# Performance work log

Hardware: AMD Instinct MI355X
Metric: run time of the kernel (lower is better)

Reference implementation:

```python
import jax, jax.numpy as jnp
import numpy as np

S = (256, 256, 256)          # MRI volume shape
N = 50000                    # number of Gaussians
T = 16                       # fixed tile edge; covers max bbox width = 2*3*sigma_max*(S-1)+2 <= 15
SIG_MIN, SIG_MAX = 0.004, 0.008  # NN-distance-based sigma range (k_sigma=1)


def setup_inputs() -> dict:
    key = jax.random.key(0)
    k1, k2, k3 = jax.random.split(key, 3)
    centers = jax.random.uniform(k1, (N, 3), dtype=jnp.float32)
    sigmas = jax.random.uniform(k2, (N,), dtype=jnp.float32, minval=SIG_MIN, maxval=SIG_MAX)
    intensities = jax.random.uniform(k3, (N,), dtype=jnp.float32)
    return {"centers": centers, "sigmas": sigmas, "intensities": intensities}


def _splat(centers, sigmas, intensities):
    dt = centers.dtype
    scale = jnp.asarray([s - 1 for s in S], dtype=dt)            # (3,) == scale_factors
    shape_f = jnp.asarray(S, dtype=dt)                           # (3,)
    shape_i = jnp.asarray(S, dtype=jnp.int32)                    # (3,)

    center_vox = centers * scale                                 # (N,3) voxel-space centers
    cutoff = 3.0 * sigmas[:, None] * scale                       # (N,3)
    # original: min_idx = max(c-cut, 0).int(); max_idx = (min(c+cut, scale)+1).int(), clipped to S
    min_idx = jnp.floor(jnp.maximum(center_vox - cutoff, 0.0)).astype(jnp.int32)          # (N,3)
    max_idx = jnp.minimum(jnp.floor(jnp.minimum(center_vox + cutoff, scale)) + 1.0,
                          shape_f).astype(jnp.int32)             # (N,3), exclusive

    ar = jnp.arange(T, dtype=jnp.int32)
    idx = min_idx[:, :, None] + ar[None, None, :]                # (N,3,T) absolute voxel idx
    valid = idx < max_idx[:, :, None]                            # (N,3,T) inside variable bbox
    idx_c = jnp.minimum(idx, shape_i[None, :, None] - 1)         # clamp for safe gather/scatter

    # grid coordinate along axis a at voxel i is i/(S_a-1) (linspace(0,1,S_a))
    coord = idx_c.astype(dt) / scale[None, :, None]              # (N,3,T)
    d = coord - centers[:, :, None]                              # (N,3,T)
    d2 = (d[:, 0, :, None, None] ** 2
          + d[:, 1, None, :, None] ** 2
          + d[:, 2, None, None, :] ** 2)                         # (N,T,T,T)
    mask = (valid[:, 0, :, None, None]
            & valid[:, 1, None, :, None]
            & valid[:, 2, None, None, :])                        # (N,T,T,T)

    inv_two_sig2 = 0.5 / (sigmas * sigmas)                       # (N,)
    contrib = intensities[:, None, None, None] * jnp.exp(-d2 * inv_two_sig2[:, None, None, None])
    contrib = jnp.where(mask, contrib, jnp.zeros((), dt))        # (N,T,T,T)

    lin = (idx_c[:, 0, :, None, None] * (S[1] * S[2])
           + idx_c[:, 1, None, :, None] * S[2]
           + idx_c[:, 2, None, None, :])                         # (N,T,T,T) flat voxel index

    vol = jnp.zeros(S[0] * S[1] * S[2], dtype=dt)
    vol = vol.at[lin.reshape(-1)].add(contrib.reshape(-1))
    return vol.reshape(S)


def reference(centers, sigmas, intensities):
    return _splat(centers, sigmas, intensities)
```

## Files before the change

kernel.cpp:

```cpp
#include <hip/hip_runtime.h>


#define NTILE  32768
#define CAP    64
#define LOG2E  1.4426950408889634f

__global__ __launch_bounds__(256) void bin_prep_kernel(
    const float* __restrict__ centers,
    const float* __restrict__ sigmas,
    const float* __restrict__ intens,
    int*    __restrict__ counts,
    float4* __restrict__ prep,
    int*    __restrict__ list,
    int N)
{
    int g = blockIdx.x * 256 + threadIdx.x;
    if (g >= N) return;
    float c0 = centers[3*g+0], c1 = centers[3*g+1], c2 = centers[3*g+2];
    float sig = sigmas[g];
    float cut = 3.0f * sig * 255.0f;
    float c[3] = {c0, c1, c2};
    int mn[3], mx[3];
    #pragma unroll
    for (int a = 0; a < 3; ++a) {
        float cv = c[a] * 255.0f;
        mn[a] = (int)floorf(fmaxf(cv - cut, 0.0f));
        mx[a] = (int)fminf(floorf(fminf(cv + cut, 255.0f)) + 1.0f, 256.0f);
    }
    float s255 = sig * 255.0f;
    float w2 = -0.5f * LOG2E / (s255 * s255);
    unsigned mnp = (unsigned)mn[0] | ((unsigned)mn[1] << 10) | ((unsigned)mn[2] << 20);
    unsigned mxp = (unsigned)mx[0] | ((unsigned)mx[1] << 10) | ((unsigned)mx[2] << 20);
    prep[2*g+0] = make_float4(c0 * 255.0f, c1 * 255.0f, c2 * 255.0f, w2);
    prep[2*g+1] = make_float4(intens[g], __uint_as_float(mnp), __uint_as_float(mxp), 0.0f);

    int t0x = mn[0] >> 3, t1x = (mx[0] - 1) >> 3;
    int t0y = mn[1] >> 3, t1y = (mx[1] - 1) >> 3;
    int t0z = mn[2] >> 3, t1z = (mx[2] - 1) >> 3;
    for (int tx = t0x; tx <= t1x; ++tx)
        for (int ty = t0y; ty <= t1y; ++ty)
            for (int tz = t0z; tz <= t1z; ++tz) {
                int t = (tx << 10) | (ty << 5) | tz;
                int slot = atomicAdd(&counts[t], 1);
                if (slot < CAP) list[t * CAP + slot] = g;
            }
}

__global__ __launch_bounds__(256) void splat_main(
    const float4* __restrict__ prep,
    const int*    __restrict__ counts,
    const int*    __restrict__ list,
    float* __restrict__ vol)
{
    int wid = threadIdx.x >> 6;
    int t   = __builtin_amdgcn_readfirstlane(blockIdx.x * 4 + wid);
    int tx = t >> 10, ty = (t >> 5) & 31, tz = t & 31;
    int ox = tx << 3, oy = ty << 3, oz = tz << 3;
    int lane = threadIdx.x & 63;
    int ly = lane >> 3, lz = lane & 7, tap = lane & 7;

    int n    = counts[t]; if (n > CAP) n = CAP;
    int base = t * CAP;

    float fyv = (float)(oy + ly);
    float fzv = (float)(oz + lz);
    float fxv = (float)(ox + tap);

    float acc[8];
    #pragma unroll
    for (int i = 0; i < 8; ++i) acc[i] = 0.0f;

    for (int k = 0; k < n; ++k) {
        int g = __builtin_amdgcn_readfirstlane(list[base + k]);
        float4 p0 = prep[2*g+0];
        float4 p1 = prep[2*g+1];

        unsigned mnp = __float_as_uint(p1.y);
        unsigned mxp = __float_as_uint(p1.z);
        int lox = max((int)( mnp        & 1023) - ox, 0), hix = min((int)( mxp        & 1023) - ox, 8);
        int loy = max((int)((mnp >> 10) & 1023) - oy, 0), hiy = min((int)((mxp >> 10) & 1023) - oy, 8);
        int loz = max((int)((mnp >> 20) & 1023) - oz, 0), hiz = min((int)((mxp >> 20) & 1023) - oz, 8);

        float dy = fyv - p0.y, dz = fzv - p0.z;
        float eyz = exp2f(fmaf(dy, dy, dz * dz) * p0.w) * p1.x;
        bool vyz = (ly >= loy) & (ly < hiy) & (lz >= loz) & (lz < hiz);
        eyz = vyz ? eyz : 0.0f;

        float dx = fxv - p0.x;
        float exv = exp2f(dx * dx * p0.w);
        bool vx = (tap >= lox) & (tap < hix);
        exv = vx ? exv : 0.0f;
        int exb = __float_as_int(exv);

        #pragma unroll
        for (int i = 0; i < 8; ++i) {
            float sx = __int_as_float(__builtin_amdgcn_readlane(exb, i));
            acc[i] = fmaf(sx, eyz, acc[i]);
        }
    }

    int ybase = ((oy + ly) << 8) + (oz + lz);
    #pragma unroll
    for (int i = 0; i < 8; ++i)
        vol[((ox + i) << 16) + ybase] = acc[i];
}

extern "C" void kernel_launch(void* const* d_in, const int* in_sizes, int n_in,
                              void* d_out, int out_size, void* d_ws, size_t ws_size,
                              hipStream_t stream) {
    const float* centers = (const float*)d_in[0];
    const float* sigmas  = (const float*)d_in[1];
    const float* intens  = (const float*)d_in[2];
    float* vol = (float*)d_out;
    const int N = in_sizes[1];

    char* ws = (char*)d_ws;
    int*    counts = (int*)ws;
    float4* prep   = (float4*)(ws + (size_t)NTILE * sizeof(int));
    int*    list   = (int*)(ws + (size_t)NTILE * sizeof(int) + (size_t)N * 32);

    hipMemsetAsync(counts, 0, NTILE * sizeof(int), stream);

    int gblocks = (N + 255) / 256;
    bin_prep_kernel<<<gblocks, 256, 0, stream>>>(centers, sigmas, intens,
                                                 counts, prep, list, N);
    splat_main<<<NTILE / 4, 256, 0, stream>>>(prep, counts, list, vol);
}
```

Measured before the change: 144.2 us.

## Precompute per-tile masks in binning and software-prefetch next Gaussian in splat loop

The binning pass now stores, for each Gaussian-tile pair, an int2 holding the Gaussian index together with precomputed x/z bit patterns and y shift amounts. The splat loop turns these into wave-wide SGPR masks applied with v_cndmask, so the per-lane bounds comparisons disappear. Intensity is folded into the exponent as log2 and added inside exp2, which removes a multiply. The next list entry and its prep data are loaded one iteration ahead to hide load latency, and CAP drops from 64 to 48, which risks overflow on dense tiles and packs the index into 16 bits, so it only works for N below 65536.

After: 141.8 us. About the same (-1.7%).

```diff
diff --git a/kernel.cpp b/kernel.cpp
--- a/kernel.cpp
+++ b/kernel.cpp
@@ -1,9 +1,11 @@
 #include <hip/hip_runtime.h>
 
 
-#define NTILE  32768
-#define CAP    64
-#define LOG2E  1.4426950408889634f
+#define NTILE 32768
+#define CAP   48
+#define LOG2E 1.4426950408889634f
+
+typedef unsigned long long ull;
 
 __global__ __launch_bounds__(256) void bin_prep_kernel(
     const float* __restrict__ centers,
@@ -11,51 +13,60 @@
     const float* __restrict__ intens,
     int*    __restrict__ counts,
     float4* __restrict__ prep,
-    int*    __restrict__ list,
+    int2*   __restrict__ list,
     int N)
 {
     int g = blockIdx.x * 256 + threadIdx.x;
     if (g >= N) return;
-    float c0 = centers[3*g+0], c1 = centers[3*g+1], c2 = centers[3*g+2];
+    float c0 = centers[3*g+0] * 255.0f;
+    float c1 = centers[3*g+1] * 255.0f;
+    float c2 = centers[3*g+2] * 255.0f;
     float sig = sigmas[g];
     float cut = 3.0f * sig * 255.0f;
-    float c[3] = {c0, c1, c2};
+    float cc[3] = {c0, c1, c2};
     int mn[3], mx[3];
     #pragma unroll
     for (int a = 0; a < 3; ++a) {
-        float cv = c[a] * 255.0f;
-        mn[a] = (int)floorf(fmaxf(cv - cut, 0.0f));
-        mx[a] = (int)fminf(floorf(fminf(cv + cut, 255.0f)) + 1.0f, 256.0f);
+        mn[a] = (int)floorf(fmaxf(cc[a] - cut, 0.0f));
+        mx[a] = (int)fminf(floorf(fminf(cc[a] + cut, 255.0f)) + 1.0f, 256.0f);
     }
     float s255 = sig * 255.0f;
     float w2 = -0.5f * LOG2E / (s255 * s255);
-    unsigned mnp = (unsigned)mn[0] | ((unsigned)mn[1] << 10) | ((unsigned)mn[2] << 20);
-    unsigned mxp = (unsigned)mx[0] | ((unsigned)mx[1] << 10) | ((unsigned)mx[2] << 20);
-    prep[2*g+0] = make_float4(c0 * 255.0f, c1 * 255.0f, c2 * 255.0f, w2);
-    prep[2*g+1] = make_float4(intens[g], __uint_as_float(mnp), __uint_as_float(mxp), 0.0f);
+    float b  = log2f(intens[g]);
+    prep[2*g+0] = make_float4(c0, c1, c2, w2);
+    prep[2*g+1] = make_float4(b, 0.0f, 0.0f, 0.0f);
 
     int t0x = mn[0] >> 3, t1x = (mx[0] - 1) >> 3;
     int t0y = mn[1] >> 3, t1y = (mx[1] - 1) >> 3;
     int t0z = mn[2] >> 3, t1z = (mx[2] - 1) >> 3;
-    for (int tx = t0x; tx <= t1x; ++tx)
-        for (int ty = t0y; ty <= t1y; ++ty)
+    for (int tx = t0x; tx <= t1x; ++tx) {
+        int lox = max(mn[0] - (tx << 3), 0), hix = min(mx[0] - (tx << 3), 8);
+        unsigned xpat = (0xFFu >> (8 - hix)) & (0xFFu << lox);
+        for (int ty = t0y; ty <= t1y; ++ty) {
+            int loy = max(mn[1] - (ty << 3), 0), hiy = min(mx[1] - (ty << 3), 8);
+            int s1 = loy << 3, s2 = 64 - (hiy << 3);
             for (int tz = t0z; tz <= t1z; ++tz) {
+                int loz = max(mn[2] - (tz << 3), 0), hiz = min(mx[2] - (tz << 3), 8);
+                unsigned zpat = (0xFFu >> (8 - hiz)) & (0xFFu << loz);
                 int t = (tx << 10) | (ty << 5) | tz;
+                int w0 = g | (int)(xpat << 16);
+                int w1 = (int)(zpat | ((unsigned)s1 << 8) | ((unsigned)s2 << 16));
                 int slot = atomicAdd(&counts[t], 1);
-                if (slot < CAP) list[t * CAP + slot] = g;
+                if (slot < CAP) list[t * CAP + slot] = make_int2(w0, w1);
             }
+        }
+    }
 }
 
 __global__ __launch_bounds__(256) void splat_main(
     const float4* __restrict__ prep,
     const int*    __restrict__ counts,
-    const int*    __restrict__ list,
+    const int2*   __restrict__ list,
     float* __restrict__ vol)
 {
     int wid = threadIdx.x >> 6;
     int t   = __builtin_amdgcn_readfirstlane(blockIdx.x * 4 + wid);
-    int tx = t >> 10, ty = (t >> 5) & 31, tz = t & 31;
-    int ox = tx << 3, oy = ty << 3, oz = tz << 3;
+    int ox = (t >> 10) << 3, oy = ((t >> 5) & 31) << 3, oz = (t & 31) << 3;
     int lane = threadIdx.x & 63;
     int ly = lane >> 3, lz = lane & 7, tap = lane & 7;
 
@@ -70,33 +81,50 @@
     #pragma unroll
     for (int i = 0; i < 8; ++i) acc[i] = 0.0f;
 
+    int2 e = (n > 0) ? list[base] : make_int2(0, 0);
+    int cw0 = __builtin_amdgcn_readfirstlane(e.x);
+    int cw1 = __builtin_amdgcn_readfirstlane(e.y);
+    int cg  = cw0 & 0xFFFF;
+    float4 cp0 = prep[2*cg+0];
+    float  cb  = prep[2*cg+1].x;
+
     for (int k = 0; k < n; ++k) {
-        int g = __builtin_amdgcn_readfirstlane(list[base + k]);
-        float4 p0 = prep[2*g+0];
-        float4 p1 = prep[2*g+1];
+        int2 en = (k + 1 < n) ? list[base + k + 1] : e;
+        int nw0 = __builtin_amdgcn_readfirstlane(en.x);
+        int nw1 = __builtin_amdgcn_readfirstlane(en.y);
+        int ng  = nw0 & 0xFFFF;
+        float4 np0 = prep[2*ng+0];
+        float  nb  = prep[2*ng+1].x;
 
-        unsigned mnp = __float_as_uint(p1.y);
-        unsigned mxp = __float_as_uint(p1.z);
-        int lox = max((int)( mnp        & 1023) - ox, 0), hix = min((int)( mxp        & 1023) - ox, 8);
-        int loy = max((int)((mnp >> 10) & 1023) - oy, 0), hiy = min((int)((mxp >> 10) & 1023) - oy, 8);
-        int loz = max((int)((mnp >> 20) & 1023) - oz, 0), hiz = min((int)((mxp >> 20) & 1023) - oz, 8);
+        unsigned xpat = ((unsigned)cw0 >> 16) & 0xFFu;
+        unsigned zpat = (unsigned)cw1 & 0xFFu;
+        int s1 = (int)(((unsigned)cw1 >> 8)  & 0xFFu);
+        int s2 = (int)(((unsigned)cw1 >> 16) & 0xFFu);
+        unsigned xm32 = xpat * 0x01010101u;
+        unsigned zm32 = zpat * 0x01010101u;
+        ull xmask = ((ull)xm32 << 32) | xm32;
+        ull ymask = ((~0ull) << s1) & ((~0ull) >> s2);
+        ull myz   = (((ull)zm32 << 32) | zm32) & ymask;
 
-        float dy = fyv - p0.y, dz = fzv - p0.z;
-        float eyz = exp2f(fmaf(dy, dy, dz * dz) * p0.w) * p1.x;
-        bool vyz = (ly >= loy) & (ly < hiy) & (lz >= loz) & (lz < hiz);
-        eyz = vyz ? eyz : 0.0f;
+        float dy = fyv - cp0.y, dz = fzv - cp0.z;
+        float d2 = fmaf(dy, dy, dz * dz);
+        float eyz = exp2f(fmaf(d2, cp0.w, cb));
+        float eyzm;
+        asm("v_cndmask_b32 %0, 0, %1, %2" : "=v"(eyzm) : "v"(eyz), "s"(myz));
 
-        float dx = fxv - p0.x;
-        float exv = exp2f(dx * dx * p0.w);
-        bool vx = (tap >= lox) & (tap < hix);
-        exv = vx ? exv : 0.0f;
-        int exb = __float_as_int(exv);
+        float dx = fxv - cp0.x;
+        float ex = exp2f(dx * dx * cp0.w);
+        float exm;
+        asm("v_cndmask_b32 %0, 0, %1, %2" : "=v"(exm) : "v"(ex), "s"(xmask));
+        int exb = __float_as_int(exm);
 
         #pragma unroll
         for (int i = 0; i < 8; ++i) {
             float sx = __int_as_float(__builtin_amdgcn_readlane(exb, i));
-            acc[i] = fmaf(sx, eyz, acc[i]);
+            acc[i] = fmaf(sx, eyzm, acc[i]);
         }
+
+        cw0 = nw0; cw1 = nw1; cp0 = np0; cb = nb; e = en;
     }
 
     int ybase = ((oy + ly) << 8) + (oz + lz);
@@ -117,7 +145,7 @@
     char* ws = (char*)d_ws;
     int*    counts = (int*)ws;
     float4* prep   = (float4*)(ws + (size_t)NTILE * sizeof(int));
-    int*    list   = (int*)(ws + (size_t)NTILE * sizeof(int) + (size_t)N * 32);
+    int2*   list   = (int2*)(ws + (size_t)NTILE * sizeof(int) + (size_t)N * 32);
 
     hipMemsetAsync(counts, 0, NTILE * sizeof(int), stream);
 
```

## Store per-tile Gaussian records with precomputed x-weights and masks in bin lists

Applied to the files above, without the earlier changes.

The binning kernel now writes a 64-byte record per (tile, Gaussian) pair. Each record holds the y/z center, the exponent weight, a 64-bit lane validity mask, and the eight x-axis exponentials with intensity already folded in. The splat kernel therefore skips the indirect prep gather, the per-iteration bbox decoding, the x exp2 and the eight readlanes, and masks with a single cndmask. The main loop is also software-pipelined three records deep. In exchange each binned Gaussian costs 16x more list memory and write bandwidth, and CAP drops to 48, which risks overflow on dense tiles.

New measurement: 140.5 us. 1.03x faster.

```diff
diff --git a/kernel.cpp b/kernel.cpp
--- a/kernel.cpp
+++ b/kernel.cpp
@@ -1,103 +1,128 @@
 #include <hip/hip_runtime.h>
 
 
-#define NTILE  32768
-#define CAP    64
-#define LOG2E  1.4426950408889634f
+#define NTILE 32768
+#define CAP   48
+#define LOG2E 1.4426950408889634f
+
+typedef unsigned long long ull;
+
+struct __align__(16) Pair {
+    unsigned mlo, mhi;
+    float cy, cz, w2;
+    float ex[8];
+    unsigned pad[3];
+};
 
 __global__ __launch_bounds__(256) void bin_prep_kernel(
     const float* __restrict__ centers,
     const float* __restrict__ sigmas,
     const float* __restrict__ intens,
-    int*    __restrict__ counts,
-    float4* __restrict__ prep,
-    int*    __restrict__ list,
+    int*  __restrict__ counts,
+    Pair* __restrict__ list,
     int N)
 {
     int g = blockIdx.x * 256 + threadIdx.x;
     if (g >= N) return;
-    float c0 = centers[3*g+0], c1 = centers[3*g+1], c2 = centers[3*g+2];
+    float cx = centers[3*g+0] * 255.0f;
+    float cy = centers[3*g+1] * 255.0f;
+    float cz = centers[3*g+2] * 255.0f;
     float sig = sigmas[g];
     float cut = 3.0f * sig * 255.0f;
-    float c[3] = {c0, c1, c2};
+    float cc[3] = {cx, cy, cz};
     int mn[3], mx[3];
     #pragma unroll
     for (int a = 0; a < 3; ++a) {
-        float cv = c[a] * 255.0f;
-        mn[a] = (int)floorf(fmaxf(cv - cut, 0.0f));
-        mx[a] = (int)fminf(floorf(fminf(cv + cut, 255.0f)) + 1.0f, 256.0f);
+        mn[a] = (int)floorf(fmaxf(cc[a] - cut, 0.0f));
+        mx[a] = (int)fminf(floorf(fminf(cc[a] + cut, 255.0f)) + 1.0f, 256.0f);
     }
     float s255 = sig * 255.0f;
     float w2 = -0.5f * LOG2E / (s255 * s255);
-    unsigned mnp = (unsigned)mn[0] | ((unsigned)mn[1] << 10) | ((unsigned)mn[2] << 20);
-    unsigned mxp = (unsigned)mx[0] | ((unsigned)mx[1] << 10) | ((unsigned)mx[2] << 20);
-    prep[2*g+0] = make_float4(c0 * 255.0f, c1 * 255.0f, c2 * 255.0f, w2);
-    prep[2*g+1] = make_float4(intens[g], __uint_as_float(mnp), __uint_as_float(mxp), 0.0f);
+    float inten = intens[g];
 
     int t0x = mn[0] >> 3, t1x = (mx[0] - 1) >> 3;
     int t0y = mn[1] >> 3, t1y = (mx[1] - 1) >> 3;
     int t0z = mn[2] >> 3, t1z = (mx[2] - 1) >> 3;
-    for (int tx = t0x; tx <= t1x; ++tx)
-        for (int ty = t0y; ty <= t1y; ++ty)
+    for (int tx = t0x; tx <= t1x; ++tx) {
+        int ox = tx << 3;
+        int lox = max(mn[0] - ox, 0), hix = min(mx[0] - ox, 8);
+        float ex[8];
+        #pragma unroll
+        for (int i = 0; i < 8; ++i) {
+            float d = (float)(ox + i) - cx;
+            float v = exp2f(d * d * w2) * inten;
+            ex[i] = (i >= lox && i < hix) ? v : 0.0f;
+        }
+        for (int ty = t0y; ty <= t1y; ++ty) {
+            int oy = ty << 3;
+            int loy = max(mn[1] - oy, 0), hiy = min(mx[1] - oy, 8);
+            ull ym = ((~0ull) << (loy << 3)) & ((~0ull) >> (64 - (hiy << 3)));
             for (int tz = t0z; tz <= t1z; ++tz) {
+                int oz = tz << 3;
+                int loz = max(mn[2] - oz, 0), hiz = min(mx[2] - oz, 8);
+                unsigned zpat = (0xFFu >> (8 - hiz)) & (0xFFu << loz);
+                ull m = (zpat * 0x0101010101010101ull) & ym;
                 int t = (tx << 10) | (ty << 5) | tz;
                 int slot = atomicAdd(&counts[t], 1);
-                if (slot < CAP) list[t * CAP + slot] = g;
+                if (slot < CAP) {
+                    int4* q = (int4*)&list[t * CAP + slot];
+                    q[0] = make_int4((int)(unsigned)m, (int)(unsigned)(m >> 32),
+                                     __float_as_int(cy), __float_as_int(cz));
+                    q[1] = make_int4(__float_as_int(w2), __float_as_int(ex[0]),
+                                     __float_as_int(ex[1]), __float_as_int(ex[2]));
+                    q[2] = make_int4(__float_as_int(ex[3]), __float_as_int(ex[4]),
+                                     __float_as_int(ex[5]), __float_as_int(ex[6]));
+                    q[3] = make_int4(__float_as_int(ex[7]), 0, 0, 0);
+                }
             }
+        }
+    }
 }
 
 __global__ __launch_bounds__(256) void splat_main(
-    const float4* __restrict__ prep,
-    const int*    __restrict__ counts,
-    const int*    __restrict__ list,
+    const int*  __restrict__ counts,
+    const Pair* __restrict__ list,
     float* __restrict__ vol)
 {
     int wid = threadIdx.x >> 6;
     int t   = __builtin_amdgcn_readfirstlane(blockIdx.x * 4 + wid);
-    int tx = t >> 10, ty = (t >> 5) & 31, tz = t & 31;
-    int ox = tx << 3, oy = ty << 3, oz = tz << 3;
+    int ox = (t >> 10) << 3, oy = ((t >> 5) & 31) << 3, oz = (t & 31) << 3;
     int lane = threadIdx.x & 63;
-    int ly = lane >> 3, lz = lane & 7, tap = lane & 7;
+    int ly = lane >> 3, lz = lane & 7;
 
-    int n    = counts[t]; if (n > CAP) n = CAP;
-    int base = t * CAP;
+    int n = counts[t]; if (n > CAP) n = CAP;
+    const Pair* base = list + t * CAP;
 
-    float fyv = (float)(oy + ly);
-    float fzv = (float)(oz + lz);
-    float fxv = (float)(ox + tap);
+    float fy = (float)(oy + ly);
+    float fz = (float)(oz + lz);
 
     float acc[8];
     #pragma unroll
     for (int i = 0; i < 8; ++i) acc[i] = 0.0f;
 
-    for (int k = 0; k < n; ++k) {
-        int g = __builtin_amdgcn_readfirstlane(list[base + k]);
-        float4 p0 = prep[2*g+0];
-        float4 p1 = prep[2*g+1];
+    auto body = [&](const Pair& p) {
+        float dy = fy - p.cy, dz = fz - p.cz;
+        float e  = exp2f(fmaf(dy, dy, dz * dz) * p.w2);
+        ull m = ((ull)p.mhi << 32) | (ull)p.mlo;
+        float em;
+        asm("v_cndmask_b32 %0, 0, %1, %2" : "=v"(em) : "v"(e), "s"(m));
+        #pragma unroll
+        for (int i = 0; i < 8; ++i)
+            acc[i] = fmaf(p.ex[i], em, acc[i]);
+    };
 
-        unsigned mnp = __float_as_uint(p1.y);
-        unsigned mxp = __float_as_uint(p1.z);
-        int lox = max((int)( mnp        & 1023) - ox, 0), hix = min((int)( mxp        & 1023) - ox, 8);
-        int loy = max((int)((mnp >> 10) & 1023) - oy, 0), hiy = min((int)((mxp >> 10) & 1023) - oy, 8);
-        int loz = max((int)((mnp >> 20) & 1023) - oz, 0), hiz = min((int)((mxp >> 20) & 1023) - oz, 8);
-
-        float dy = fyv - p0.y, dz = fzv - p0.z;
-        float eyz = exp2f(fmaf(dy, dy, dz * dz) * p0.w) * p1.x;
-        bool vyz = (ly >= loy) & (ly < hiy) & (lz >= loz) & (lz < hiz);
-        eyz = vyz ? eyz : 0.0f;
-
-        float dx = fxv - p0.x;
-        float exv = exp2f(dx * dx * p0.w);
-        bool vx = (tap >= lox) & (tap < hix);
-        exv = vx ? exv : 0.0f;
-        int exb = __float_as_int(exv);
-
-        #pragma unroll
-        for (int i = 0; i < 8; ++i) {
-            float sx = __int_as_float(__builtin_amdgcn_readlane(exb, i));
-            acc[i] = fmaf(sx, eyz, acc[i]);
-        }
+    Pair p0 = base[0], p1 = base[1], p2 = base[2];
+    int k = 0;
+    for (; k + 3 <= n; k += 3) {
+        Pair a = base[k + 3];
+        Pair b = base[k + 4];
+        Pair c = base[k + 5];
+        body(p0); body(p1); body(p2);
+        p0 = a; p1 = b; p2 = c;
     }
+    if (k     < n) body(p0);
+    if (k + 1 < n) body(p1);
+    if (k + 2 < n) body(p2);
 
     int ybase = ((oy + ly) << 8) + (oz + lz);
     #pragma unroll
@@ -115,14 +140,13 @@
     const int N = in_sizes[1];
 
     char* ws = (char*)d_ws;
-    int*    counts = (int*)ws;
-    float4* prep   = (float4*)(ws + (size_t)NTILE * sizeof(int));
-    int*    list   = (int*)(ws + (size_t)NTILE * sizeof(int) + (size_t)N * 32);
+    int*  counts = (int*)ws;
+    Pair* list   = (Pair*)(ws + (size_t)NTILE * sizeof(int));
 
     hipMemsetAsync(counts, 0, NTILE * sizeof(int), stream);
 
     int gblocks = (N + 255) / 256;
     bin_prep_kernel<<<gblocks, 256, 0, stream>>>(centers, sigmas, intens,
-                                                 counts, prep, list, N);
-    splat_main<<<NTILE / 4, 256, 0, stream>>>(prep, counts, list, vol);
+                                                 counts, list, N);
+    splat_main<<<NTILE / 4, 256, 0, stream>>>(counts, list, vol);
 }
```
